# Performance work log

Measured on AMD Instinct MI355X. Metric: run time of the kernel, lower is better.

The kernel has to match this reference:

```python
import jax, jax.numpy as jnp
import numpy as np

D = 1024   # dim_embedding
H = 16     # n_head
HD = D // H


def setup_inputs() -> dict:
    key = jax.random.key(0)
    ks = jax.random.split(key, 5)
    B, T = 2, 2048
    x = jax.random.normal(ks[0], (B, T, D), dtype=jnp.float32)
    e = jax.random.normal(ks[1], (B, T, D), dtype=jnp.float32)
    s = 0.02
    W_en = jax.random.normal(ks[2], (D, 2 * D), dtype=jnp.float32) * s   # c_attn_en (k,v from encoder)
    W_q = jax.random.normal(ks[3], (D, D), dtype=jnp.float32) * s        # c_attn (q from decoder)
    W_o = jax.random.normal(ks[4], (D, D), dtype=jnp.float32) * s        # c_proj
    return {"x": x, "e": e, "W_en": W_en, "W_q": W_q, "W_o": W_o}


def reference(x, e, W_en, W_q, W_o):
    B, T, C = e.shape
    kv = e @ W_en                       # [B,T,2C]
    k, v = jnp.split(kv, 2, axis=-1)    # [B,T,C] each
    q = x @ W_q                         # [B,T,C]
    # reshape to heads: [B,H,T,hd]
    q = q.reshape(B, T, H, HD).transpose(0, 2, 1, 3)
    k = k.reshape(B, T, H, HD).transpose(0, 2, 1, 3)
    v = v.reshape(B, T, H, HD).transpose(0, 2, 1, 3)
    att = jnp.einsum("bhqd,bhkd->bhqk", q, k) * (1.0 / jnp.sqrt(jnp.float32(HD)))
    att = jax.nn.softmax(att, axis=-1)  # dropout=0 (eval)
    y = jnp.einsum("bhqk,bhkd->bhqd", att, v)
    y = y.transpose(0, 2, 1, 3).reshape(B, T, C)
    return y @ W_o
```

## Files before the change

kernel.cpp:

```cpp
#include <hip/hip_runtime.h>

typedef unsigned short u16;
typedef unsigned int u32;
typedef __bf16 bf16x8 __attribute__((ext_vector_type(8)));
typedef float f32x4 __attribute__((ext_vector_type(4)));
typedef float f32x16 __attribute__((ext_vector_type(16)));

#define D_EMB 1024
#define T_SEQ 2048
#define NH 16
#define HD 64

#define GLB(p) ((const __attribute__((address_space(1))) unsigned int*)(p))
#define LDSP(p) ((__attribute__((address_space(3))) unsigned int*)(p))

__device__ __forceinline__ u16 f2bf(float f) {
  union { float f; unsigned u; } c; c.f = f;
  unsigned u = c.u;
  unsigned r = (u + 0x7FFFu + ((u >> 16) & 1u)) >> 16;
  return (u16)r;
}
__device__ __forceinline__ u32 fbits(float f) {
  union { float f; unsigned u; } c; c.f = f; return c.u;
}

__global__ __launch_bounds__(256) void prep_kernel(
    const float* __restrict__ x, const float* __restrict__ e,
    const float* __restrict__ W_q, const float* __restrict__ W_en, const float* __restrict__ W_o,
    u16* __restrict__ xb, u16* __restrict__ eb,
    u16* __restrict__ Wqt, u16* __restrict__ Went, u16* __restrict__ Wot) {
  __shared__ float tile[32][33];
  const int bid = blockIdx.x, tid = threadIdx.x;
  if (bid < 8192) {
    const float* in = (bid < 4096) ? x : e;
    u16* out = (bid < 4096) ? xb : eb;
    int i = (bid & 4095) * 256 + tid;
    float4 v = reinterpret_cast<const float4*>(in)[i];
    ushort4 o;
    o.x = f2bf(v.x); o.y = f2bf(v.y); o.z = f2bf(v.z); o.w = f2bf(v.w);
    reinterpret_cast<ushort4*>(out)[i] = o;
    return;
  }
  const float* in; u16* out; int K, N, bx, by;
  int rem = bid - 8192;
  if (rem < 1024)      { in = W_q;  out = Wqt;  K = 1024; N = 1024; bx = rem & 31; by = rem >> 5; }
  else if (rem < 3072) { int r2 = rem - 1024; in = W_en; out = Went; K = 1024; N = 2048; bx = r2 & 63; by = r2 >> 6; }
  else                 { int r3 = rem - 3072; in = W_o;  out = Wot;  K = 1024; N = 1024; bx = r3 & 31; by = r3 >> 5; }
  int tx = tid & 31, ty = tid >> 5;
  int n0 = bx * 32, k0 = by * 32;
#pragma unroll
  for (int s = 0; s < 4; s++)
    tile[ty + 8 * s][tx] = in[(size_t)(k0 + ty + 8 * s) * N + n0 + tx];
  __syncthreads();
#pragma unroll
  for (int s = 0; s < 4; s++)
    out[(size_t)(n0 + ty + 8 * s) * K + k0 + tx] = f2bf(tile[tx][ty + 8 * s]);
}

__global__ __launch_bounds__(256) void proj_kernel(
    const u16* __restrict__ xb, const u16* __restrict__ eb,
    const u16* __restrict__ Wqt, const u16* __restrict__ Went,
    u16* __restrict__ qw, u16* __restrict__ kw, u16* __restrict__ vTw) {
  __shared__ u16 Al0[128 * 32], Bl0[128 * 32];
  __shared__ u16 Al1[128 * 32], Bl1[128 * 32];
  const int tid = threadIdx.x;
  const int nb = blockIdx.x, mb = blockIdx.y;
  const int wave = tid >> 6, lane = tid & 63;
  const int ln15 = lane & 15, quad = lane >> 4;
  const int wm = wave & 1, wn = wave >> 1;

  const u16* A = (nb < 8) ? xb : eb;
  const u16* Wt = (nb < 8) ? (Wqt + (size_t)nb * 128 * D_EMB)
                           : (Went + ((size_t)nb * 128 - D_EMB) * D_EMB);

  const int srow = lane >> 2, sch = lane & 3;
  const int gch = sch ^ ((srow >> 1) & 3);
  const u16* gA = A + (size_t)(mb * 128 + wave * 32 + srow) * D_EMB + gch * 8;
  const u16* gB = Wt + (size_t)(wave * 32 + srow) * D_EMB + gch * 8;

  auto stage = [&](int kb, u16* AL, u16* BL) {
    char* lA = (char*)AL + wave * 2048;
    char* lB = (char*)BL + wave * 2048;
#pragma unroll
    for (int it = 0; it < 2; it++) {
      __builtin_amdgcn_global_load_lds(GLB(gA + (size_t)it * 16 * D_EMB + kb), LDSP(lA + it * 1024), 16, 0, 0);
      __builtin_amdgcn_global_load_lds(GLB(gB + (size_t)it * 16 * D_EMB + kb), LDSP(lB + it * 1024), 16, 0, 0);
    }
  };

  f32x4 acc[4][4] = {};

  auto compute = [&](const u16* AL, const u16* BL) {
    bf16x8 af[4], bfr[4];
#pragma unroll
    for (int mt = 0; mt < 4; mt++) {
      int r = wm * 64 + mt * 16 + ln15;
      af[mt] = *reinterpret_cast<const bf16x8*>(&AL[r * 32 + ((quad ^ ((r >> 1) & 3)) * 8)]);
    }
#pragma unroll
    for (int nt = 0; nt < 4; nt++) {
      int r = wn * 64 + nt * 16 + ln15;
      bfr[nt] = *reinterpret_cast<const bf16x8*>(&BL[r * 32 + ((quad ^ ((r >> 1) & 3)) * 8)]);
    }
#pragma unroll
    for (int mt = 0; mt < 4; mt++)
#pragma unroll
      for (int nt = 0; nt < 4; nt++)
        acc[mt][nt] = __builtin_amdgcn_mfma_f32_16x16x32_bf16(af[mt], bfr[nt], acc[mt][nt], 0, 0, 0);
  };

  stage(0, Al0, Bl0);
  for (int kb = 0; kb < D_EMB; kb += 64) {
    __syncthreads();
    stage(kb + 32, Al1, Bl1);
    compute(Al0, Bl0);
    __syncthreads();
    if (kb + 64 < D_EMB) stage(kb + 64, Al0, Bl0);
    compute(Al1, Bl1);
  }

  const float QSCL = 0.125f * 1.44269504f;
#pragma unroll
  for (int mt = 0; mt < 4; mt++) {
#pragma unroll
    for (int nt = 0; nt < 4; nt++) {
#pragma unroll
      for (int i = 0; i < 4; i++) {
        int rr = mb * 128 + wm * 64 + mt * 16 + quad * 4 + i;
        int c  = nb * 128 + wn * 64 + nt * 16 + ln15;
        float v = acc[mt][nt][i];
        int b = rr >> 11, t = rr & 2047;
        if (c < D_EMB) {
          int h = c >> 6, d = c & 63;
          qw[(((size_t)(b * NH + h)) * T_SEQ + t) * HD + d] = f2bf(v * QSCL);
        } else if (c < 2 * D_EMB) {
          int cc = c - D_EMB; int h = cc >> 6, d = cc & 63;
          kw[(((size_t)(b * NH + h)) * T_SEQ + t) * HD + d] = f2bf(v);
        } else {
          int cc = c - 2 * D_EMB; int h = cc >> 6, d = cc & 63;
          vTw[(((size_t)(b * NH + h)) * HD + d) * T_SEQ + t] = f2bf(v);
        }
      }
    }
  }
}

__global__ __launch_bounds__(256) void attn_kernel(
    const u16* __restrict__ q, const u16* __restrict__ k,
    const u16* __restrict__ vT, u16* __restrict__ y) {
  __shared__ u16 Kl0[64][64], Vl0[64][64];
  __shared__ u16 Kl1[64][64], Vl1[64][64];

  const int bh = blockIdx.y;
  const int qt = blockIdx.x;
  const int tid = threadIdx.x;
  const int wave = tid >> 6, lane = tid & 63;
  const int q32 = lane & 31, hi = lane >> 5;
  const int b = bh >> 4, h = bh & 15;

  const int pq = (q32 & 19) | ((q32 & 8) >> 1) | ((q32 & 4) << 1);
  const int pq7 = pq & 7;

  const int qrow = qt * 128 + wave * 32 + q32;
  const u16* qbase = q + ((size_t)bh * T_SEQ + qrow) * HD;
  bf16x8 qf[4];
#pragma unroll
  for (int s = 0; s < 4; s++)
    qf[s] = *reinterpret_cast<const bf16x8*>(qbase + s * 16 + hi * 8);

  f32x16 o2[2] = {};
  float lp = 0.f;

  const int srow = (lane >> 3) & 7;
  const int gch  = (lane & 7) ^ srow;
  const u16* kg0 = k  + ((size_t)bh * T_SEQ + wave * 16 + srow) * HD + gch * 8;
  const u16* vg0 = vT + ((size_t)bh * HD + wave * 16 + srow) * T_SEQ + gch * 8;

  auto issue_dma = [&](int t, u16 (*KL)[64], u16 (*VL)[64]) {
    char* klb = (char*)KL + wave * 2048;
    char* vlb = (char*)VL + wave * 2048;
    const u16* kp = kg0 + (size_t)t * 64 * HD;
    const u16* vp = vg0 + t * 64;
    __builtin_amdgcn_global_load_lds(GLB(kp),             LDSP(klb),        16, 0, 0);
    __builtin_amdgcn_global_load_lds(GLB(kp + 8 * HD),    LDSP(klb + 1024), 16, 0, 0);
    __builtin_amdgcn_global_load_lds(GLB(vp),             LDSP(vlb),        16, 0, 0);
    __builtin_amdgcn_global_load_lds(GLB(vp + 8 * T_SEQ), LDSP(vlb + 1024), 16, 0, 0);
  };

  auto body = [&](const u16 (*KL)[64], const u16 (*VL)[64]) {
    f32x16 s2[2] = {};
#pragma unroll
    for (int s = 0; s < 4; s++)
#pragma unroll
      for (int kt2 = 0; kt2 < 2; kt2++) {
        int r = kt2 * 32 + pq;
        bf16x8 kf = *reinterpret_cast<const bf16x8*>(&KL[r][(((s * 2 + hi) ^ pq7) * 8)]);
        s2[kt2] = __builtin_amdgcn_mfma_f32_32x32x16_bf16(kf, qf[s], s2[kt2], 0, 0, 0);
      }

#pragma unroll
    for (int s = 0; s < 4; s++) {
      const int kt2 = s >> 1;
      const int g0 = (2 * s) & 3;
      float e0 = __builtin_amdgcn_exp2f(s2[kt2][4 * g0 + 0]);
      float e1 = __builtin_amdgcn_exp2f(s2[kt2][4 * g0 + 1]);
      float e2 = __builtin_amdgcn_exp2f(s2[kt2][4 * g0 + 2]);
      float e3 = __builtin_amdgcn_exp2f(s2[kt2][4 * g0 + 3]);
      float e4 = __builtin_amdgcn_exp2f(s2[kt2][4 * g0 + 4]);
      float e5 = __builtin_amdgcn_exp2f(s2[kt2][4 * g0 + 5]);
      float e6 = __builtin_amdgcn_exp2f(s2[kt2][4 * g0 + 6]);
      float e7 = __builtin_amdgcn_exp2f(s2[kt2][4 * g0 + 7]);
      lp += ((e0 + e1) + (e2 + e3)) + ((e4 + e5) + (e6 + e7));
      u32 w0 = __builtin_amdgcn_perm(fbits(e1), fbits(e0), 0x07060302u);
      u32 w1 = __builtin_amdgcn_perm(fbits(e3), fbits(e2), 0x07060302u);
      u32 w2 = __builtin_amdgcn_perm(fbits(e5), fbits(e4), 0x07060302u);
      u32 w3 = __builtin_amdgcn_perm(fbits(e7), fbits(e6), 0x07060302u);
      union { u32 w[4]; bf16x8 v; } pu;
      pu.w[0] = w0; pu.w[1] = w1; pu.w[2] = w2; pu.w[3] = w3;
      bf16x8 pf = pu.v;
#pragma unroll
      for (int dt = 0; dt < 2; dt++) {
        int r = dt * 32 + q32;
        bf16x8 vf = *reinterpret_cast<const bf16x8*>(&VL[r][(((s * 2 + hi) ^ (r & 7)) * 8)]);
        o2[dt] = __builtin_amdgcn_mfma_f32_32x32x16_bf16(vf, pf, o2[dt], 0, 0, 0);
      }
    }
  };

  issue_dma(0, Kl0, Vl0);
  for (int t = 0; t < 32; t += 2) {
    __syncthreads();
    issue_dma(t + 1, Kl1, Vl1);
    body(Kl0, Vl0);
    __syncthreads();
    if (t + 2 < 32) issue_dma(t + 2, Kl0, Vl0);
    body(Kl1, Vl1);
  }

  lp += __shfl_xor(lp, 32, 64);
  const float inv = 1.0f / lp;

  const size_t ybase = ((size_t)b * T_SEQ + qrow) * D_EMB + h * 64;
#pragma unroll
  for (int dt = 0; dt < 2; dt++)
#pragma unroll
    for (int g = 0; g < 4; g++) {
      u16 b0 = f2bf(o2[dt][4 * g + 0] * inv), b1 = f2bf(o2[dt][4 * g + 1] * inv);
      u16 b2 = f2bf(o2[dt][4 * g + 2] * inv), b3 = f2bf(o2[dt][4 * g + 3] * inv);
      u32 dw0 = (u32)b0 | ((u32)b1 << 16);
      u32 dw1 = (u32)b2 | ((u32)b3 << 16);
      *reinterpret_cast<uint2*>(&y[ybase + dt * 32 + 8 * g + 4 * hi]) = make_uint2(dw0, dw1);
    }
}

__global__ __launch_bounds__(256) void oproj_kernel(
    const u16* __restrict__ yw, const u16* __restrict__ Wot, float* __restrict__ out) {
  __shared__ u16 Al0[64 * 32], Al1[64 * 32];
  __shared__ u16 Bl0[128 * 32], Bl1[128 * 32];
  const int tid = threadIdx.x;
  const int nb = blockIdx.x, mb = blockIdx.y;
  const int wave = tid >> 6, lane = tid & 63;
  const int ln15 = lane & 15, quad = lane >> 4;
  const int wm = wave & 1, wn = wave >> 1;

  const int srow = lane >> 2, sch = lane & 3;
  const int gch = sch ^ ((srow >> 1) & 3);
  const u16* gA = yw  + (size_t)(mb * 64 + wave * 16 + srow) * D_EMB + gch * 8;
  const u16* gB = Wot + (size_t)(nb * 128 + wave * 32 + srow) * D_EMB + gch * 8;

  auto stage = [&](int kb, u16* AL, u16* BL) {
    char* lA = (char*)AL + wave * 1024;
    char* lB = (char*)BL + wave * 2048;
    __builtin_amdgcn_global_load_lds(GLB(gA + kb), LDSP(lA), 16, 0, 0);
#pragma unroll
    for (int it = 0; it < 2; it++)
      __builtin_amdgcn_global_load_lds(GLB(gB + (size_t)it * 16 * D_EMB + kb), LDSP(lB + it * 1024), 16, 0, 0);
  };

  f32x4 acc[2][4] = {};

  auto compute = [&](const u16* AL, const u16* BL) {
    bf16x8 af[2], bfr[4];
#pragma unroll
    for (int mt = 0; mt < 2; mt++) {
      int r = wm * 32 + mt * 16 + ln15;
      af[mt] = *reinterpret_cast<const bf16x8*>(&AL[r * 32 + ((quad ^ ((r >> 1) & 3)) * 8)]);
    }
#pragma unroll
    for (int nt = 0; nt < 4; nt++) {
      int r = wn * 64 + nt * 16 + ln15;
      bfr[nt] = *reinterpret_cast<const bf16x8*>(&BL[r * 32 + ((quad ^ ((r >> 1) & 3)) * 8)]);
    }
#pragma unroll
    for (int mt = 0; mt < 2; mt++)
#pragma unroll
      for (int nt = 0; nt < 4; nt++)
        acc[mt][nt] = __builtin_amdgcn_mfma_f32_16x16x32_bf16(af[mt], bfr[nt], acc[mt][nt], 0, 0, 0);
  };

  stage(0, Al0, Bl0);
  for (int kb = 0; kb < D_EMB; kb += 64) {
    __syncthreads();
    stage(kb + 32, Al1, Bl1);
    compute(Al0, Bl0);
    __syncthreads();
    if (kb + 64 < D_EMB) stage(kb + 64, Al0, Bl0);
    compute(Al1, Bl1);
  }

#pragma unroll
  for (int mt = 0; mt < 2; mt++)
#pragma unroll
    for (int nt = 0; nt < 4; nt++)
#pragma unroll
      for (int i = 0; i < 4; i++) {
        int rr = mb * 64 + wm * 32 + mt * 16 + quad * 4 + i;
        int c  = nb * 128 + wn * 64 + nt * 16 + ln15;
        out[(size_t)rr * D_EMB + c] = acc[mt][nt][i];
      }
}

extern "C" void kernel_launch(void* const* d_in, const int* in_sizes, int n_in,
                              void* d_out, int out_size, void* d_ws, size_t ws_size,
                              hipStream_t stream) {
  const float* x    = (const float*)d_in[0];
  const float* e    = (const float*)d_in[1];
  const float* W_en = (const float*)d_in[2];
  const float* W_q  = (const float*)d_in[3];
  const float* W_o  = (const float*)d_in[4];
  float* out = (float*)d_out;

  char* w = (char*)d_ws;
  u16* xb   = (u16*)(w);
  u16* eb   = (u16*)(w + (8u  << 20));
  u16* Wqt  = (u16*)(w + (16u << 20));
  u16* Went = (u16*)(w + (18u << 20));
  u16* Wot  = (u16*)(w + (22u << 20));
  u16* qw   = (u16*)(w + (24u << 20));
  u16* kw   = (u16*)(w + (32u << 20));
  u16* vT   = (u16*)(w + (40u << 20));
  u16* yw   = (u16*)(w + (48u << 20));

  prep_kernel<<<12288, 256, 0, stream>>>(x, e, W_q, W_en, W_o, xb, eb, Wqt, Went, Wot);
  proj_kernel<<<dim3(24, 32), 256, 0, stream>>>(xb, eb, Wqt, Went, qw, kw, vT);
  attn_kernel<<<dim3(T_SEQ / 128, 32), 256, 0, stream>>>(qw, kw, vT, yw);
  oproj_kernel<<<dim3(8, 64), 256, 0, stream>>>(yw, Wot, out);
}
```

Before: 198.0 us.

## Triple-buffer LDS staging with explicit vmcnt waits in GEMM and attention kernels

Replaces the double-buffered global-to-LDS pipelines in the projection, attention and output-projection kernels with three-stage ring buffers. Waits use explicit s_waitcnt vmcnt counts plus raw barriers, so two loads stay in flight while one buffer is consumed. The GEMMs also split fragment loads from MFMA issue and raise wave priority during the MFMA block. The cost is more LDS per block, which may lower occupancy, and the hand-counted vmcnt values become fragile if the number of loads per stage changes.

```diff
diff --git a/kernel.cpp b/kernel.cpp
--- a/kernel.cpp
+++ b/kernel.cpp
@@ -13,6 +13,8 @@
 
 #define GLB(p) ((const __attribute__((address_space(1))) unsigned int*)(p))
 #define LDSP(p) ((__attribute__((address_space(3))) unsigned int*)(p))
+#define VMCNT(n) asm volatile("s_waitcnt vmcnt(" #n ")" ::: "memory")
+#define LGKM0() asm volatile("s_waitcnt lgkmcnt(0)" ::: "memory")
 
 __device__ __forceinline__ u16 f2bf(float f) {
   union { float f; unsigned u; } c; c.f = f;
@@ -61,8 +63,7 @@
     const u16* __restrict__ xb, const u16* __restrict__ eb,
     const u16* __restrict__ Wqt, const u16* __restrict__ Went,
     u16* __restrict__ qw, u16* __restrict__ kw, u16* __restrict__ vTw) {
-  __shared__ u16 Al0[128 * 32], Bl0[128 * 32];
-  __shared__ u16 Al1[128 * 32], Bl1[128 * 32];
+  __shared__ u16 Al[3][128 * 32], Bl[3][128 * 32];
   const int tid = threadIdx.x;
   const int nb = blockIdx.x, mb = blockIdx.y;
   const int wave = tid >> 6, lane = tid & 63;
@@ -89,9 +90,9 @@
   };
 
   f32x4 acc[4][4] = {};
-
-  auto compute = [&](const u16* AL, const u16* BL) {
-    bf16x8 af[4], bfr[4];
+  bf16x8 af[4], bfr[4];
+
+  auto ldfrag = [&](const u16* AL, const u16* BL) {
 #pragma unroll
     for (int mt = 0; mt < 4; mt++) {
       int r = wm * 64 + mt * 16 + ln15;
@@ -102,22 +103,37 @@
       int r = wn * 64 + nt * 16 + ln15;
       bfr[nt] = *reinterpret_cast<const bf16x8*>(&BL[r * 32 + ((quad ^ ((r >> 1) & 3)) * 8)]);
     }
+  };
+  auto domfma = [&]() {
+    __builtin_amdgcn_s_setprio(1);
 #pragma unroll
     for (int mt = 0; mt < 4; mt++)
 #pragma unroll
       for (int nt = 0; nt < 4; nt++)
         acc[mt][nt] = __builtin_amdgcn_mfma_f32_16x16x32_bf16(af[mt], bfr[nt], acc[mt][nt], 0, 0, 0);
-  };
-
-  stage(0, Al0, Bl0);
-  for (int kb = 0; kb < D_EMB; kb += 64) {
-    __syncthreads();
-    stage(kb + 32, Al1, Bl1);
-    compute(Al0, Bl0);
-    __syncthreads();
-    if (kb + 64 < D_EMB) stage(kb + 64, Al0, Bl0);
-    compute(Al1, Bl1);
-  }
+    __builtin_amdgcn_s_setprio(0);
+  };
+
+  stage(0,  Al[0], Bl[0]);
+  stage(32, Al[1], Bl[1]);
+  stage(64, Al[2], Bl[2]);
+  u16 *cA = Al[0], *cB = Bl[0], *nA = Al[1], *nB = Bl[1], *mA = Al[2], *mB = Bl[2];
+
+  for (int kb = 0; kb < 928; kb += 32) {
+    VMCNT(8);
+    __builtin_amdgcn_s_barrier();
+    ldfrag(cA, cB);
+    LGKM0();
+    __builtin_amdgcn_s_barrier();
+    stage(kb + 96, cA, cB);
+    domfma();
+    u16* t;
+    t = cA; cA = nA; nA = mA; mA = t;
+    t = cB; cB = nB; nB = mB; mB = t;
+  }
+  VMCNT(8); __builtin_amdgcn_s_barrier(); ldfrag(cA, cB); domfma();
+  VMCNT(4); __builtin_amdgcn_s_barrier(); ldfrag(nA, nB); domfma();
+  VMCNT(0); __builtin_amdgcn_s_barrier(); ldfrag(mA, mB); domfma();
 
   const float QSCL = 0.125f * 1.44269504f;
 #pragma unroll
@@ -148,8 +164,7 @@
 __global__ __launch_bounds__(256) void attn_kernel(
     const u16* __restrict__ q, const u16* __restrict__ k,
     const u16* __restrict__ vT, u16* __restrict__ y) {
-  __shared__ u16 Kl0[64][64], Vl0[64][64];
-  __shared__ u16 Kl1[64][64], Vl1[64][64];
+  __shared__ u16 Kl[3][64][64], Vl[3][64][64];
 
   const int bh = blockIdx.y;
   const int qt = blockIdx.x;
@@ -227,15 +242,27 @@
     }
   };
 
-  issue_dma(0, Kl0, Vl0);
-  for (int t = 0; t < 32; t += 2) {
-    __syncthreads();
-    issue_dma(t + 1, Kl1, Vl1);
-    body(Kl0, Vl0);
-    __syncthreads();
-    if (t + 2 < 32) issue_dma(t + 2, Kl0, Vl0);
-    body(Kl1, Vl1);
-  }
+  issue_dma(0, Kl[0], Vl[0]);
+  issue_dma(1, Kl[1], Vl[1]);
+  issue_dma(2, Kl[2], Vl[2]);
+  u16 (*cK)[64] = Kl[0]; u16 (*cV)[64] = Vl[0];
+  u16 (*nK)[64] = Kl[1]; u16 (*nV)[64] = Vl[1];
+  u16 (*mK)[64] = Kl[2]; u16 (*mV)[64] = Vl[2];
+
+  for (int t = 0; t < 29; t++) {
+    VMCNT(8);
+    __builtin_amdgcn_s_barrier();
+    body(cK, cV);
+    LGKM0();
+    __builtin_amdgcn_s_barrier();
+    issue_dma(t + 3, cK, cV);
+    u16 (*tp)[64];
+    tp = cK; cK = nK; nK = mK; mK = tp;
+    tp = cV; cV = nV; nV = mV; mV = tp;
+  }
+  VMCNT(8); __builtin_amdgcn_s_barrier(); body(cK, cV);
+  VMCNT(4); __builtin_amdgcn_s_barrier(); body(nK, nV);
+  VMCNT(0); __builtin_amdgcn_s_barrier(); body(mK, mV);
 
   lp += __shfl_xor(lp, 32, 64);
   const float inv = 1.0f / lp;
@@ -255,8 +282,7 @@
 
 __global__ __launch_bounds__(256) void oproj_kernel(
     const u16* __restrict__ yw, const u16* __restrict__ Wot, float* __restrict__ out) {
-  __shared__ u16 Al0[64 * 32], Al1[64 * 32];
-  __shared__ u16 Bl0[128 * 32], Bl1[128 * 32];
+  __shared__ u16 Al[3][64 * 32], Bl[3][128 * 32];
   const int tid = threadIdx.x;
   const int nb = blockIdx.x, mb = blockIdx.y;
   const int wave = tid >> 6, lane = tid & 63;
@@ -278,9 +304,9 @@
   };
 
   f32x4 acc[2][4] = {};
-
-  auto compute = [&](const u16* AL, const u16* BL) {
-    bf16x8 af[2], bfr[4];
+  bf16x8 af[2], bfr[4];
+
+  auto ldfrag = [&](const u16* AL, const u16* BL) {
 #pragma unroll
     for (int mt = 0; mt < 2; mt++) {
       int r = wm * 32 + mt * 16 + ln15;
@@ -291,22 +317,37 @@
       int r = wn * 64 + nt * 16 + ln15;
       bfr[nt] = *reinterpret_cast<const bf16x8*>(&BL[r * 32 + ((quad ^ ((r >> 1) & 3)) * 8)]);
     }
+  };
+  auto domfma = [&]() {
+    __builtin_amdgcn_s_setprio(1);
 #pragma unroll
     for (int mt = 0; mt < 2; mt++)
 #pragma unroll
       for (int nt = 0; nt < 4; nt++)
         acc[mt][nt] = __builtin_amdgcn_mfma_f32_16x16x32_bf16(af[mt], bfr[nt], acc[mt][nt], 0, 0, 0);
-  };
-
-  stage(0, Al0, Bl0);
-  for (int kb = 0; kb < D_EMB; kb += 64) {
-    __syncthreads();
-    stage(kb + 32, Al1, Bl1);
-    compute(Al0, Bl0);
-    __syncthreads();
-    if (kb + 64 < D_EMB) stage(kb + 64, Al0, Bl0);
-    compute(Al1, Bl1);
-  }
+    __builtin_amdgcn_s_setprio(0);
+  };
+
+  stage(0,  Al[0], Bl[0]);
+  stage(32, Al[1], Bl[1]);
+  stage(64, Al[2], Bl[2]);
+  u16 *cA = Al[0], *cB = Bl[0], *nA = Al[1], *nB = Bl[1], *mA = Al[2], *mB = Bl[2];
+
+  for (int kb = 0; kb < 928; kb += 32) {
+    VMCNT(6);
+    __builtin_amdgcn_s_barrier();
+    ldfrag(cA, cB);
+    LGKM0();
+    __builtin_amdgcn_s_barrier();
+    stage(kb + 96, cA, cB);
+    domfma();
+    u16* t;
+    t = cA; cA = nA; nA = mA; mA = t;
+    t = cB; cB = nB; nB = mB; mB = t;
+  }
+  VMCNT(6); __builtin_amdgcn_s_barrier(); ldfrag(cA, cB); domfma();
+  VMCNT(3); __builtin_amdgcn_s_barrier(); ldfrag(nA, nB); domfma();
+  VMCNT(0); __builtin_amdgcn_s_barrier(); ldfrag(mA, mB); domfma();
 
 #pragma unroll
   for (int mt = 0; mt < 2; mt++)
```

Result: no change. 195.9 us (-1.0%).
